# Performance work log

Measured on AMD Instinct MI355X. Metric: run time of the kernel, lower is better.

Reference implementation:

```python
import jax, jax.numpy as jnp
import numpy as np
import math

B, S, T = 128, 600, 200
ENC = 512      # listener_hidden_size * 2
P = 128        # projection_size (hardcoded 128 in forward)
E = 256        # embedding_dim
H = 512        # hidden_dim
V = 31         # vocab_size
SOS = 1


def setup_inputs() -> dict:
    key = jax.random.key(0)
    ks = iter(jax.random.split(key, 40))
    def rn(shape, scale):
        return (jax.random.normal(next(ks), shape, dtype=jnp.float32) * scale)
    inp = {}
    inp['x'] = rn((B, S, ENC), 1.0)
    inp['y'] = jax.random.randint(next(ks), (B, T), 0, V)
    inp['enc_lens'] = jax.random.randint(next(ks), (B,), 100, S + 1)
    # xavier-normal initial hidden/cell states (as in the torch forward)
    xav = math.sqrt(2.0 / (B + H))
    inp['h0'] = rn((3, B, H), xav)
    inp['c0'] = rn((3, B, H), xav)
    # embedding, padding_idx=0 row zeroed
    emb = rn((V, E), 0.05)
    inp['emb'] = emb.at[0].set(0.0)
    # LSTM cells: cell0 input E+P, cells 1,2 input H. torch init: U(-1/sqrt(H), 1/sqrt(H))
    def uni(shape):
        lim = 1.0 / math.sqrt(H)
        return jax.random.uniform(next(ks), shape, jnp.float32, -lim, lim)
    inp['W_ih0'] = uni((4 * H, E + P)); inp['W_hh0'] = uni((4 * H, H))
    inp['b_ih0'] = uni((4 * H,));       inp['b_hh0'] = uni((4 * H,))
    inp['W_ih1'] = uni((4 * H, H));     inp['W_hh1'] = uni((4 * H, H))
    inp['b_ih1'] = uni((4 * H,));       inp['b_hh1'] = uni((4 * H,))
    inp['W_ih2'] = uni((4 * H, H));     inp['W_hh2'] = uni((4 * H, H))
    inp['b_ih2'] = uni((4 * H,));       inp['b_hh2'] = uni((4 * H,))
    # attention projections
    inp['KW_w'] = rn((P, ENC), 0.03); inp['KW_b'] = jnp.zeros((P,), jnp.float32)
    inp['VW_w'] = rn((P, ENC), 0.03); inp['VW_b'] = jnp.zeros((P,), jnp.float32)
    inp['QW_w'] = rn((P, H), 0.03);   inp['QW_b'] = jnp.zeros((P,), jnp.float32)
    # CDN head
    inp['out_w'] = rn((E, H + P), 0.03); inp['out_b'] = jnp.zeros((E,), jnp.float32)
    inp['char_w'] = rn((V, E), 0.05);    inp['char_b'] = jnp.zeros((V,), jnp.float32)
    return inp


def _lstm_cell(x, h, c, W_ih, W_hh, b_ih, b_hh):
    g = x @ W_ih.T + b_ih + h @ W_hh.T + b_hh
    i, f, gg, o = jnp.split(g, 4, axis=-1)
    c = jax.nn.sigmoid(f) * c + jax.nn.sigmoid(i) * jnp.tanh(gg)
    h = jax.nn.sigmoid(o) * jnp.tanh(c)
    return h, c


def reference(x, y, enc_lens, h0, c0, emb,
              W_ih0, W_hh0, b_ih0, b_hh0,
              W_ih1, W_hh1, b_ih1, b_hh1,
              W_ih2, W_hh2, b_ih2, b_hh2,
              KW_w, KW_b, VW_w, VW_b, QW_w, QW_b,
              out_w, out_b, char_w, char_b):
    # set_key_value
    key_ = x @ KW_w.T + KW_b      # (B,S,P)
    value = x @ VW_w.T + VW_b     # (B,S,P)
    mask = jnp.arange(S)[None, :] >= enc_lens[:, None]  # (B,S) True = masked
    scale = 1.0 / math.sqrt(P)

    cells = ((W_ih0, W_hh0, b_ih0, b_hh0),
             (W_ih1, W_hh1, b_ih1, b_hh1),
             (W_ih2, W_hh2, b_ih2, b_hh2))

    # teacher forcing ratio 1: input token at step t is SOS (t=0) then y[:, t-1]
    tokens = jnp.concatenate([jnp.full((B, 1), SOS, dtype=y.dtype), y[:, :-1]], axis=1)
    tokens = tokens.T  # (T,B)

    def step(carry, tok):
        hs, cs, ctx = carry
        inp = jnp.concatenate([emb[tok], ctx], axis=1)  # (B, E+P)
        new_h, new_c = [], []
        for i in range(3):
            h, c = _lstm_cell(inp, hs[i], cs[i], *cells[i])
            new_h.append(h); new_c.append(c)
            inp = h
        rnn_out = inp  # (B,H)
        q = rnn_out @ QW_w.T + QW_b                              # (B,P)
        logits = jnp.einsum('bsp,bp->bs', key_, q) * scale       # (B,S)
        logits = jnp.where(mask, -jnp.inf, logits)
        w = jax.nn.softmax(logits, axis=1)                        # (B,S)
        ctx = jnp.einsum('bs,bsp->bp', w, value)                  # (B,P)
        cdn_in = jnp.concatenate([rnn_out, ctx], axis=1)          # (B,H+P)
        hidden = jax.nn.gelu(cdn_in @ out_w.T + out_b, approximate=False)
        pred = hidden @ char_w.T + char_b                         # (B,V)
        return (jnp.stack(new_h), jnp.stack(new_c), ctx), (pred, w)

    ctx0 = jnp.zeros((B, P), dtype=x.dtype)
    _, (preds, attn) = jax.lax.scan(step, (h0, c0, ctx0), tokens)
    raw_outputs = jnp.transpose(preds, (1, 0, 2))      # (B,T,V)
    attention_plot = jnp.transpose(attn, (1, 0, 2))    # (B,T,S)
    return raw_outputs, attention_plot
```

## Files before the change

### kernel.cpp

```cpp
#include <hip/hip_runtime.h>
#include <hip/hip_fp16.h>


#define Bc 128
#define Sc 600
#define Tc 200
#define ENCc 512
#define Pc 128
#define Ec 256
#define Hc 512
#define Vc 31

__device__ __forceinline__ float sigmoidf_(float x) { return 1.f / (1.f + expf(-x)); }

__global__ __launch_bounds__(256) void init_kernel(
    const float* __restrict__ h0, const float* __restrict__ c0,
    float* __restrict__ hbuf, float* __restrict__ cst, float* __restrict__ ctx)
{
  const int i = blockIdx.x * 256 + threadIdx.x;
  if (i < 3 * Bc * Hc) { hbuf[i] = h0[i]; cst[i] = c0[i]; }
  if (i < Bc * Pc) ctx[i] = 0.f;
}

__global__ __launch_bounds__(256) void kv_kernel(
    const float* __restrict__ x,
    const float* __restrict__ KW_w, const float* __restrict__ KW_b,
    const float* __restrict__ VW_w, const float* __restrict__ VW_b,
    __half* __restrict__ key16, __half* __restrict__ val16)
{
  const int r0 = blockIdx.x * 32;
  const int tid = threadIdx.x;
  const bool isv = tid >= 128;
  const int p = tid & 127;
  const float* __restrict__ W = isv ? VW_w : KW_w;
  float acc[32];
#pragma unroll
  for (int r = 0; r < 32; ++r) acc[r] = 0.f;
  __shared__ float xs[32][64];
  for (int c = 0; c < 8; ++c) {
    const int k0 = c * 64;
    __syncthreads();
#pragma unroll
    for (int i = 0; i < 2; ++i) {
      const int e = i * 256 + tid;
      const int row = e >> 4, c4 = e & 15;
      *(float4*)(&xs[row][c4 * 4]) =
          *(const float4*)(x + (size_t)(r0 + row) * ENCc + k0 + c4 * 4);
    }
    __syncthreads();
    const float* wr = W + (size_t)p * ENCc + k0;
#pragma unroll
    for (int kk = 0; kk < 16; ++kk) {
      const float4 w4 = *(const float4*)(wr + kk * 4);
#pragma unroll
      for (int r = 0; r < 32; ++r) {
        const float4 xv = *(const float4*)(&xs[r][kk * 4]);
        acc[r] += w4.x * xv.x + w4.y * xv.y + w4.z * xv.z + w4.w * xv.w;
      }
    }
  }
  const float bias = isv ? VW_b[p] : KW_b[p];
  __half* __restrict__ dst = isv ? val16 : key16;
#pragma unroll
  for (int r = 0; r < 32; ++r)
    dst[(size_t)(r0 + r) * Pc + p] = __float2half(acc[r] + bias);
}

#define CHUNK_COMPUTE(W0_, W1_, W2_, W3_, K0_)                                   \
  {                                                                              \
    _Pragma("unroll") for (int m = 0; m < 4; ++m)                                \
    {                                                                            \
      const int kl = kg * 4 + m * 32;                                            \
      const float4 a0 = *(const float4*)((W0_) + (K0_) + kl);                    \
      const float4 a1 = *(const float4*)((W1_) + (K0_) + kl);                    \
      const float4 a2 = *(const float4*)((W2_) + (K0_) + kl);                    \
      const float4 a3 = *(const float4*)((W3_) + (K0_) + kl);                    \
      _Pragma("unroll") for (int bb = 0; bb < 4; ++bb)                           \
      {                                                                          \
        const float4 xv = *(const float4*)(&xs[bq * 4 + bb][kl]);                \
        acc[0][bb] += a0.x * xv.x + a0.y * xv.y + a0.z * xv.z + a0.w * xv.w;     \
        acc[1][bb] += a1.x * xv.x + a1.y * xv.y + a1.z * xv.z + a1.w * xv.w;     \
        acc[2][bb] += a2.x * xv.x + a2.y * xv.y + a2.z * xv.z + a2.w * xv.w;     \
        acc[3][bb] += a3.x * xv.x + a3.y * xv.y + a3.z * xv.z + a3.w * xv.w;     \
      }                                                                          \
    }                                                                            \
  }

template <int CELL>
__global__ __launch_bounds__(512) void cell_kernel(
    const float* __restrict__ W_ih, const float* __restrict__ W_hh,
    const float* __restrict__ b_ih, const float* __restrict__ b_hh,
    const float* __restrict__ emb, const int* __restrict__ y,
    const float* __restrict__ ctx,
    const float* __restrict__ hold, float* __restrict__ hnew,
    float* __restrict__ cst, const int t)
{
  constexpr int K1 = (CELL == 0) ? 384 : 512;
  const int u0 = blockIdx.x * 8, b0 = blockIdx.y * 32;
  const int tid = threadIdx.x;
  const int kg = tid & 7, bq = (tid >> 3) & 7, jq = tid >> 6;
  const int u = u0 + jq;
  float acc[4][4] = {{0.f,0.f,0.f,0.f},{0.f,0.f,0.f,0.f},{0.f,0.f,0.f,0.f},{0.f,0.f,0.f,0.f}};
  __shared__ float xs[32][132];

  {
    const float* w0 = W_ih + (size_t)(u)        * K1;
    const float* w1 = W_ih + (size_t)(u + 512)  * K1;
    const float* w2 = W_ih + (size_t)(u + 1024) * K1;
    const float* w3 = W_ih + (size_t)(u + 1536) * K1;
#pragma unroll
    for (int c = 0; c < K1 / 128; ++c) {
      const int k0 = c * 128;
      __syncthreads();
#pragma unroll
      for (int i = 0; i < 2; ++i) {
        const int e = i * 512 + tid;
        const int row = e >> 5, c4 = e & 31;
        const int k = k0 + c4 * 4;
        const int b = b0 + row;
        float4 v;
        if (CELL == 0) {
          if (k < 256) {
            const int tok = (t == 0) ? 1 : y[b * Tc + t - 1];
            v = *(const float4*)(emb + (size_t)tok * Ec + k);
          } else {
            v = *(const float4*)(ctx + (size_t)b * Pc + (k - 256));
          }
        } else {
          v = *(const float4*)(hnew + (size_t)(CELL - 1) * (Bc * Hc) + (size_t)b * Hc + k);
        }
        *(float4*)(&xs[row][c4 * 4]) = v;
      }
      __syncthreads();
      CHUNK_COMPUTE(w0, w1, w2, w3, k0)
    }
  }
  {
    const float* w0 = W_hh + (size_t)(u)        * Hc;
    const float* w1 = W_hh + (size_t)(u + 512)  * Hc;
    const float* w2 = W_hh + (size_t)(u + 1024) * Hc;
    const float* w3 = W_hh + (size_t)(u + 1536) * Hc;
    const float* hsrc = hold + (size_t)CELL * (Bc * Hc);
#pragma unroll
    for (int c = 0; c < 4; ++c) {
      const int k0 = c * 128;
      __syncthreads();
#pragma unroll
      for (int i = 0; i < 2; ++i) {
        const int e = i * 512 + tid;
        const int row = e >> 5, c4 = e & 31;
        *(float4*)(&xs[row][c4 * 4]) =
            *(const float4*)(hsrc + (size_t)(b0 + row) * Hc + k0 + c4 * 4);
      }
      __syncthreads();
      CHUNK_COMPUTE(w0, w1, w2, w3, k0)
    }
  }
#pragma unroll
  for (int g = 0; g < 4; ++g) {
#pragma unroll
    for (int bb = 0; bb < 4; ++bb) {
      float v = acc[g][bb];
      v += __shfl_xor(v, 1);
      v += __shfl_xor(v, 2);
      v += __shfl_xor(v, 4);
      acc[g][bb] = v;
    }
  }
  if (kg == 0) {
    const float bi = b_ih[u]        + b_hh[u];
    const float bf = b_ih[u + 512]  + b_hh[u + 512];
    const float bg = b_ih[u + 1024] + b_hh[u + 1024];
    const float bo = b_ih[u + 1536] + b_hh[u + 1536];
    float* hn = hnew + (size_t)CELL * (Bc * Hc);
    float* cs = cst  + (size_t)CELL * (Bc * Hc);
#pragma unroll
    for (int bb = 0; bb < 4; ++bb) {
      const int b = b0 + bq * 4 + bb;
      const int idx = b * Hc + u;
      const float ig = sigmoidf_(acc[0][bb] + bi);
      const float fg = sigmoidf_(acc[1][bb] + bf);
      const float gg = tanhf(acc[2][bb] + bg);
      const float og = sigmoidf_(acc[3][bb] + bo);
      const float cn = fg * cs[idx] + ig * gg;
      cs[idx] = cn;
      hn[idx] = og * tanhf(cn);
    }
  }
}

__device__ __forceinline__ float wave_max_(float v) {
#pragma unroll
  for (int o = 32; o; o >>= 1) v = fmaxf(v, __shfl_xor(v, o));
  return v;
}
__device__ __forceinline__ float wave_sum_(float v) {
#pragma unroll
  for (int o = 32; o; o >>= 1) v += __shfl_xor(v, o);
  return v;
}

__global__ __launch_bounds__(256) void attn_cdn_kernel(
    const float* __restrict__ hnew,
    const __half* __restrict__ key16, const __half* __restrict__ val16,
    const int* __restrict__ enc_lens,
    const float* __restrict__ QW_w, const float* __restrict__ QW_b,
    const float* __restrict__ out_w, const float* __restrict__ out_b,
    const float* __restrict__ char_w, const float* __restrict__ char_b,
    float* __restrict__ ctx_out, float* __restrict__ raw_out,
    float* __restrict__ attn_out, const int t)
{
  const int b = blockIdx.x, tid = threadIdx.x;
  __shared__ float h2s[Hc], qs[Pc], wsm[Sc], ctxs[Pc], hid[Ec];
  __shared__ float s_red[4];
  const float* h2 = hnew + 2 * (Bc * Hc) + (size_t)b * Hc;
  for (int i = tid; i < Hc; i += 256) h2s[i] = h2[i];
  __syncthreads();
  if (tid < Pc) {
    const float* wr = QW_w + (size_t)tid * Hc;
    float a = QW_b[tid];
#pragma unroll 8
    for (int k = 0; k < Hc; k += 4) {
      const float4 w = *(const float4*)(wr + k);
      a += w.x * h2s[k] + w.y * h2s[k + 1] + w.z * h2s[k + 2] + w.w * h2s[k + 3];
    }
    qs[tid] = a;
  }
  __syncthreads();
  const int len = enc_lens[b];
  float lmax = -3.0e38f;
  for (int s = tid; s < Sc; s += 256) {
    if (s < len) {
      const __half* kr = key16 + ((size_t)(b * Sc + s)) * Pc;
      float a = 0.f;
#pragma unroll 16
      for (int p = 0; p < Pc; p += 4) {
        const float2 k01 = __half22float2(*(const __half2*)(kr + p));
        const float2 k23 = __half22float2(*(const __half2*)(kr + p + 2));
        a += k01.x * qs[p] + k01.y * qs[p + 1] + k23.x * qs[p + 2] + k23.y * qs[p + 3];
      }
      const float sc = a * 0.08838834764831845f;
      wsm[s] = sc;
      lmax = fmaxf(lmax, sc);
    }
  }
  float wm = wave_max_(lmax);
  if ((tid & 63) == 0) s_red[tid >> 6] = wm;
  __syncthreads();
  const float mx = fmaxf(fmaxf(s_red[0], s_red[1]), fmaxf(s_red[2], s_red[3]));
  __syncthreads();
  float lsum = 0.f;
  for (int s = tid; s < Sc; s += 256)
    if (s < len) { const float e = expf(wsm[s] - mx); wsm[s] = e; lsum += e; }
  float ws_ = wave_sum_(lsum);
  if ((tid & 63) == 0) s_red[tid >> 6] = ws_;
  __syncthreads();
  const float inv = 1.f / (s_red[0] + s_red[1] + s_red[2] + s_red[3]);
  float* ap = attn_out + ((size_t)(b * Tc + t)) * Sc;
  for (int s = tid; s < Sc; s += 256) {
    const float w = (s < len) ? wsm[s] * inv : 0.f;
    wsm[s] = w;
    ap[s] = w;
  }
  __syncthreads();
  if (tid < Pc) {
    const __half* vp = val16 + ((size_t)b * Sc) * Pc + tid;
    float a = 0.f;
#pragma unroll 4
    for (int s = 0; s < len; ++s) a += wsm[s] * __half2float(vp[(size_t)s * Pc]);
    ctxs[tid] = a;
    ctx_out[b * Pc + tid] = a;
  }
  __syncthreads();
  {
    const float* wr = out_w + (size_t)tid * (Hc + Pc);
    float a = out_b[tid];
#pragma unroll 8
    for (int k = 0; k < Hc; k += 4) {
      const float4 w = *(const float4*)(wr + k);
      a += w.x * h2s[k] + w.y * h2s[k + 1] + w.z * h2s[k + 2] + w.w * h2s[k + 3];
    }
#pragma unroll 8
    for (int k = 0; k < Pc; k += 4) {
      const float4 w = *(const float4*)(wr + Hc + k);
      a += w.x * ctxs[k] + w.y * ctxs[k + 1] + w.z * ctxs[k + 2] + w.w * ctxs[k + 3];
    }
    hid[tid] = 0.5f * a * (1.f + erff(a * 0.70710678118654752440f));
  }
  __syncthreads();
  if (tid < Vc) {
    const float* wr = char_w + (size_t)tid * Ec;
    float a = char_b[tid];
#pragma unroll 8
    for (int k = 0; k < Ec; k += 4) {
      const float4 w = *(const float4*)(wr + k);
      a += w.x * hid[k] + w.y * hid[k + 1] + w.z * hid[k + 2] + w.w * hid[k + 3];
    }
    raw_out[((size_t)(b * Tc + t)) * Vc + tid] = a;
  }
}

extern "C" void kernel_launch(void* const* d_in, const int* in_sizes, int n_in,
                              void* d_out, int out_size, void* d_ws, size_t ws_size,
                              hipStream_t stream) {
  (void)in_sizes; (void)n_in; (void)out_size; (void)ws_size;
  const float* x      = (const float*)d_in[0];
  const int*   y      = (const int*)  d_in[1];
  const int*   enc    = (const int*)  d_in[2];
  const float* h0     = (const float*)d_in[3];
  const float* c0     = (const float*)d_in[4];
  const float* emb    = (const float*)d_in[5];
  const float* W_ih0  = (const float*)d_in[6];
  const float* W_hh0  = (const float*)d_in[7];
  const float* b_ih0  = (const float*)d_in[8];
  const float* b_hh0  = (const float*)d_in[9];
  const float* W_ih1  = (const float*)d_in[10];
  const float* W_hh1  = (const float*)d_in[11];
  const float* b_ih1  = (const float*)d_in[12];
  const float* b_hh1  = (const float*)d_in[13];
  const float* W_ih2  = (const float*)d_in[14];
  const float* W_hh2  = (const float*)d_in[15];
  const float* b_ih2  = (const float*)d_in[16];
  const float* b_hh2  = (const float*)d_in[17];
  const float* KW_w   = (const float*)d_in[18];
  const float* KW_b   = (const float*)d_in[19];
  const float* VW_w   = (const float*)d_in[20];
  const float* VW_b   = (const float*)d_in[21];
  const float* QW_w   = (const float*)d_in[22];
  const float* QW_b   = (const float*)d_in[23];
  const float* out_w  = (const float*)d_in[24];
  const float* out_b  = (const float*)d_in[25];
  const float* char_w = (const float*)d_in[26];
  const float* char_b = (const float*)d_in[27];

  float* out  = (float*)d_out;
  float* raw  = out;
  float* attn = out + 793600;

  char* ws = (char*)d_ws;
  __half* key16 = (__half*)(ws);
  __half* val16 = (__half*)(ws + 19660800);
  float*  hbuf  = (float*) (ws + 39321600);
  float*  cst   = (float*) (ws + 39321600 + 1572864);
  float*  ctx   = (float*) (ws + 39321600 + 1572864 + 786432);

  init_kernel<<<768, 256, 0, stream>>>(h0, c0, hbuf, cst, ctx);
  kv_kernel<<<2400, 256, 0, stream>>>(x, KW_w, KW_b, VW_w, VW_b, key16, val16);

  for (int t = 0; t < Tc; ++t) {
    float* hold = hbuf + (size_t)(t & 1) * (3 * Bc * Hc);
    float* hnew = hbuf + (size_t)((t & 1) ^ 1) * (3 * Bc * Hc);
    cell_kernel<0><<<dim3(64, 4), 512, 0, stream>>>(W_ih0, W_hh0, b_ih0, b_hh0,
                                                    emb, y, ctx, hold, hnew, cst, t);
    cell_kernel<1><<<dim3(64, 4), 512, 0, stream>>>(W_ih1, W_hh1, b_ih1, b_hh1,
                                                    emb, y, ctx, hold, hnew, cst, t);
    cell_kernel<2><<<dim3(64, 4), 512, 0, stream>>>(W_ih2, W_hh2, b_ih2, b_hh2,
                                                    emb, y, ctx, hold, hnew, cst, t);
    attn_cdn_kernel<<<128, 256, 0, stream>>>(hnew, key16, val16, enc,
                                             QW_w, QW_b, out_w, out_b, char_w, char_b,
                                             ctx, raw, attn, t);
  }
}
```

Baseline: 30.94 ms.

## Fuse per-timestep cell and attention launches into one persistent cooperative kernel

Replaces the 800 per-timestep kernel launches with a single cooperative persistent kernel of 256 blocks. The blocks step through the three LSTM cells and the attention/CDN phase, separated by a hand-rolled flag-based grid barrier. The layer-0 input (embedding plus context) is now built into a staging buffer by idle blocks during the attention phase, and the attention block size doubles to 512 threads with the context reduction split over two halves. The aim is to remove launch overhead and gaps between kernels. In exchange it adds spin-wait barrier latency and depends on all 256 blocks being co-resident.

```diff
diff --git a/kernel.cpp b/kernel.cpp
--- a/kernel.cpp
+++ b/kernel.cpp
@@ -10,16 +10,23 @@
 #define Ec 256
 #define Hc 512
 #define Vc 31
+#define BHc (Bc * Hc)
 
 __device__ __forceinline__ float sigmoidf_(float x) { return 1.f / (1.f + expf(-x)); }
 
 __global__ __launch_bounds__(256) void init_kernel(
     const float* __restrict__ h0, const float* __restrict__ c0,
-    float* __restrict__ hbuf, float* __restrict__ cst, float* __restrict__ ctx)
+    const float* __restrict__ emb,
+    float* __restrict__ hbuf, float* __restrict__ cst,
+    float* __restrict__ xin0, unsigned* __restrict__ bar)
 {
   const int i = blockIdx.x * 256 + threadIdx.x;
-  if (i < 3 * Bc * Hc) { hbuf[i] = h0[i]; cst[i] = c0[i]; }
-  if (i < Bc * Pc) ctx[i] = 0.f;
+  if (i < 3 * BHc) { hbuf[i] = h0[i]; cst[i] = c0[i]; }
+  if (i < Bc * 384) {
+    const int k = i % 384;
+    xin0[i] = (k < 256) ? emb[256 + k] : 0.f;
+  }
+  if (i < 257) bar[i] = 0u;
 }
 
 __global__ __launch_bounds__(256) void kv_kernel(
@@ -64,6 +71,26 @@
 #pragma unroll
   for (int r = 0; r < 32; ++r)
     dst[(size_t)(r0 + r) * Pc + p] = __float2half(acc[r] + bias);
+}
+
+__device__ __forceinline__ void grid_bar(unsigned* __restrict__ arrive,
+                                         unsigned* __restrict__ go, unsigned it) {
+  __syncthreads();
+  if (threadIdx.x == 0)
+    __hip_atomic_store(&arrive[blockIdx.x], it, __ATOMIC_RELEASE, __HIP_MEMORY_SCOPE_AGENT);
+  if (blockIdx.x == 0) {
+    if (threadIdx.x < 256) {
+      while (__hip_atomic_load(&arrive[threadIdx.x], __ATOMIC_ACQUIRE,
+                               __HIP_MEMORY_SCOPE_AGENT) < it) {}
+    }
+    __syncthreads();
+    if (threadIdx.x == 0)
+      __hip_atomic_store(go, it, __ATOMIC_RELEASE, __HIP_MEMORY_SCOPE_AGENT);
+  }
+  if (threadIdx.x == 0) {
+    while (__hip_atomic_load(go, __ATOMIC_ACQUIRE, __HIP_MEMORY_SCOPE_AGENT) < it) {}
+  }
+  __syncthreads();
 }
 
 #define CHUNK_COMPUTE(W0_, W1_, W2_, W3_, K0_)                                   \
@@ -86,22 +113,20 @@
     }                                                                            \
   }
 
-template <int CELL>
-__global__ __launch_bounds__(512) void cell_kernel(
+template <int K1>
+__device__ __forceinline__ void cell_phase(
     const float* __restrict__ W_ih, const float* __restrict__ W_hh,
     const float* __restrict__ b_ih, const float* __restrict__ b_hh,
-    const float* __restrict__ emb, const int* __restrict__ y,
-    const float* __restrict__ ctx,
+    const float* __restrict__ xin,
     const float* __restrict__ hold, float* __restrict__ hnew,
-    float* __restrict__ cst, const int t)
+    float* __restrict__ cs, float* __restrict__ smem)
 {
-  constexpr int K1 = (CELL == 0) ? 384 : 512;
-  const int u0 = blockIdx.x * 8, b0 = blockIdx.y * 32;
+  const int u0 = (blockIdx.x >> 2) * 8, b0 = (blockIdx.x & 3) * 32;
   const int tid = threadIdx.x;
   const int kg = tid & 7, bq = (tid >> 3) & 7, jq = tid >> 6;
   const int u = u0 + jq;
   float acc[4][4] = {{0.f,0.f,0.f,0.f},{0.f,0.f,0.f,0.f},{0.f,0.f,0.f,0.f},{0.f,0.f,0.f,0.f}};
-  __shared__ float xs[32][132];
+  float (*xs)[132] = (float (*)[132])smem;
 
   {
     const float* w0 = W_ih + (size_t)(u)        * K1;
@@ -116,20 +141,8 @@
       for (int i = 0; i < 2; ++i) {
         const int e = i * 512 + tid;
         const int row = e >> 5, c4 = e & 31;
-        const int k = k0 + c4 * 4;
-        const int b = b0 + row;
-        float4 v;
-        if (CELL == 0) {
-          if (k < 256) {
-            const int tok = (t == 0) ? 1 : y[b * Tc + t - 1];
-            v = *(const float4*)(emb + (size_t)tok * Ec + k);
-          } else {
-            v = *(const float4*)(ctx + (size_t)b * Pc + (k - 256));
-          }
-        } else {
-          v = *(const float4*)(hnew + (size_t)(CELL - 1) * (Bc * Hc) + (size_t)b * Hc + k);
-        }
-        *(float4*)(&xs[row][c4 * 4]) = v;
+        *(float4*)(&xs[row][c4 * 4]) =
+            *(const float4*)(xin + (size_t)(b0 + row) * K1 + k0 + c4 * 4);
       }
       __syncthreads();
       CHUNK_COMPUTE(w0, w1, w2, w3, k0)
@@ -140,7 +153,6 @@
     const float* w1 = W_hh + (size_t)(u + 512)  * Hc;
     const float* w2 = W_hh + (size_t)(u + 1024) * Hc;
     const float* w3 = W_hh + (size_t)(u + 1536) * Hc;
-    const float* hsrc = hold + (size_t)CELL * (Bc * Hc);
 #pragma unroll
     for (int c = 0; c < 4; ++c) {
       const int k0 = c * 128;
@@ -150,7 +162,7 @@
         const int e = i * 512 + tid;
         const int row = e >> 5, c4 = e & 31;
         *(float4*)(&xs[row][c4 * 4]) =
-            *(const float4*)(hsrc + (size_t)(b0 + row) * Hc + k0 + c4 * 4);
+            *(const float4*)(hold + (size_t)(b0 + row) * Hc + k0 + c4 * 4);
       }
       __syncthreads();
       CHUNK_COMPUTE(w0, w1, w2, w3, k0)
@@ -172,8 +184,6 @@
     const float bf = b_ih[u + 512]  + b_hh[u + 512];
     const float bg = b_ih[u + 1024] + b_hh[u + 1024];
     const float bo = b_ih[u + 1536] + b_hh[u + 1536];
-    float* hn = hnew + (size_t)CELL * (Bc * Hc);
-    float* cs = cst  + (size_t)CELL * (Bc * Hc);
 #pragma unroll
     for (int bb = 0; bb < 4; ++bb) {
       const int b = b0 + bq * 4 + bb;
@@ -184,7 +194,7 @@
       const float og = sigmoidf_(acc[3][bb] + bo);
       const float cn = fg * cs[idx] + ig * gg;
       cs[idx] = cn;
-      hn[idx] = og * tanhf(cn);
+      hnew[idx] = og * tanhf(cn);
     }
   }
 }
@@ -200,21 +210,37 @@
   return v;
 }
 
-__global__ __launch_bounds__(256) void attn_cdn_kernel(
-    const float* __restrict__ hnew,
+__device__ __forceinline__ void attn_phase(
+    const float* __restrict__ h2,
     const __half* __restrict__ key16, const __half* __restrict__ val16,
     const int* __restrict__ enc_lens,
     const float* __restrict__ QW_w, const float* __restrict__ QW_b,
     const float* __restrict__ out_w, const float* __restrict__ out_b,
     const float* __restrict__ char_w, const float* __restrict__ char_b,
-    float* __restrict__ ctx_out, float* __restrict__ raw_out,
-    float* __restrict__ attn_out, const int t)
+    const float* __restrict__ emb, const int* __restrict__ y,
+    float* __restrict__ xin0,
+    float* __restrict__ raw_out, float* __restrict__ attn_out,
+    float* __restrict__ smem, const int t)
 {
-  const int b = blockIdx.x, tid = threadIdx.x;
-  __shared__ float h2s[Hc], qs[Pc], wsm[Sc], ctxs[Pc], hid[Ec];
-  __shared__ float s_red[4];
-  const float* h2 = hnew + 2 * (Bc * Hc) + (size_t)b * Hc;
-  for (int i = tid; i < Hc; i += 256) h2s[i] = h2[i];
+  const int tid = threadIdx.x;
+  if (blockIdx.x >= 128) {
+    const int b = blockIdx.x - 128;
+    if (tid < 256) {
+      const int tok = y[b * Tc + t];
+      xin0[b * 384 + tid] = emb[tok * Ec + tid];
+    }
+    return;
+  }
+  const int b = blockIdx.x;
+  float* h2s  = smem;
+  float* qs   = smem + 512;
+  float* wsm  = smem + 640;
+  float* ctxs = smem + 1240;
+  float* hid  = smem + 1368;
+  float* red  = smem + 1632;
+  float* part = smem + 1648;
+
+  h2s[tid] = h2[(size_t)b * Hc + tid];
   __syncthreads();
   if (tid < Pc) {
     const float* wr = QW_w + (size_t)tid * Hc;
@@ -229,7 +255,7 @@
   __syncthreads();
   const int len = enc_lens[b];
   float lmax = -3.0e38f;
-  for (int s = tid; s < Sc; s += 256) {
+  for (int s = tid; s < Sc; s += 512) {
     if (s < len) {
       const __half* kr = key16 + ((size_t)(b * Sc + s)) * Pc;
       float a = 0.f;
@@ -245,34 +271,47 @@
     }
   }
   float wm = wave_max_(lmax);
-  if ((tid & 63) == 0) s_red[tid >> 6] = wm;
-  __syncthreads();
-  const float mx = fmaxf(fmaxf(s_red[0], s_red[1]), fmaxf(s_red[2], s_red[3]));
+  if ((tid & 63) == 0) red[tid >> 6] = wm;
+  __syncthreads();
+  float mx = red[0];
+#pragma unroll
+  for (int w = 1; w < 8; ++w) mx = fmaxf(mx, red[w]);
   __syncthreads();
   float lsum = 0.f;
-  for (int s = tid; s < Sc; s += 256)
+  for (int s = tid; s < Sc; s += 512)
     if (s < len) { const float e = expf(wsm[s] - mx); wsm[s] = e; lsum += e; }
   float ws_ = wave_sum_(lsum);
-  if ((tid & 63) == 0) s_red[tid >> 6] = ws_;
-  __syncthreads();
-  const float inv = 1.f / (s_red[0] + s_red[1] + s_red[2] + s_red[3]);
+  if ((tid & 63) == 0) red[tid >> 6] = ws_;
+  __syncthreads();
+  float tot = 0.f;
+#pragma unroll
+  for (int w = 0; w < 8; ++w) tot += red[w];
+  const float inv = 1.f / tot;
   float* ap = attn_out + ((size_t)(b * Tc + t)) * Sc;
-  for (int s = tid; s < Sc; s += 256) {
+  for (int s = tid; s < Sc; s += 512) {
     const float w = (s < len) ? wsm[s] * inv : 0.f;
     wsm[s] = w;
     ap[s] = w;
   }
   __syncthreads();
-  if (tid < Pc) {
-    const __half* vp = val16 + ((size_t)b * Sc) * Pc + tid;
+  if (tid < 256) {
+    const int p = tid & 127, hf = tid >> 7;
+    const int s_beg = hf * 300;
+    const int s_end = (len < (hf + 1) * 300) ? ((len > s_beg) ? len : s_beg) : (hf + 1) * 300;
+    const __half* vp = val16 + ((size_t)b * Sc) * Pc + p;
     float a = 0.f;
 #pragma unroll 4
-    for (int s = 0; s < len; ++s) a += wsm[s] * __half2float(vp[(size_t)s * Pc]);
+    for (int s = s_beg; s < s_end; ++s) a += wsm[s] * __half2float(vp[(size_t)s * Pc]);
+    part[hf * 128 + p] = a;
+  }
+  __syncthreads();
+  if (tid < Pc) {
+    const float a = part[tid] + part[128 + tid];
     ctxs[tid] = a;
-    ctx_out[b * Pc + tid] = a;
-  }
-  __syncthreads();
-  {
+    xin0[b * 384 + 256 + tid] = a;
+  }
+  __syncthreads();
+  if (tid < Ec) {
     const float* wr = out_w + (size_t)tid * (Hc + Pc);
     float a = out_b[tid];
 #pragma unroll 8
@@ -297,6 +336,40 @@
       a += w.x * hid[k] + w.y * hid[k + 1] + w.z * hid[k + 2] + w.w * hid[k + 3];
     }
     raw_out[((size_t)(b * Tc + t)) * Vc + tid] = a;
+  }
+}
+
+struct PParams {
+  const float *W_ih0, *W_hh0, *b_ih0, *b_hh0;
+  const float *W_ih1, *W_hh1, *b_ih1, *b_hh1;
+  const float *W_ih2, *W_hh2, *b_ih2, *b_hh2;
+  const float *emb; const int *y; const int *enc;
+  const float *QW_w, *QW_b, *out_w, *out_b, *char_w, *char_b;
+  const __half *key16, *val16;
+  float *hbuf, *cst, *xin0;
+  unsigned *bar_arrive, *bar_go;
+  float *raw, *attn;
+};
+
+__global__ __launch_bounds__(512, 2) void persist_kernel(PParams p) {
+  __shared__ float smem[32 * 132];
+  unsigned it = 0;
+  for (int t = 0; t < Tc; ++t) {
+    const float* hold = p.hbuf + (size_t)(t & 1) * (3 * BHc);
+    float* hnew = p.hbuf + (size_t)((t & 1) ^ 1) * (3 * BHc);
+    cell_phase<384>(p.W_ih0, p.W_hh0, p.b_ih0, p.b_hh0, p.xin0,
+                    hold, hnew, p.cst, smem);
+    grid_bar(p.bar_arrive, p.bar_go, ++it);
+    cell_phase<512>(p.W_ih1, p.W_hh1, p.b_ih1, p.b_hh1, hnew,
+                    hold + BHc, hnew + BHc, p.cst + BHc, smem);
+    grid_bar(p.bar_arrive, p.bar_go, ++it);
+    cell_phase<512>(p.W_ih2, p.W_hh2, p.b_ih2, p.b_hh2, hnew + BHc,
+                    hold + 2 * BHc, hnew + 2 * BHc, p.cst + 2 * BHc, smem);
+    grid_bar(p.bar_arrive, p.bar_go, ++it);
+    attn_phase(hnew + 2 * BHc, p.key16, p.val16, p.enc, p.QW_w, p.QW_b,
+               p.out_w, p.out_b, p.char_w, p.char_b, p.emb, p.y,
+               p.xin0, p.raw, p.attn, smem, t);
+    grid_bar(p.bar_arrive, p.bar_go, ++it);
   }
 }
 
@@ -338,26 +411,29 @@
   float* attn = out + 793600;
 
   char* ws = (char*)d_ws;
-  __half* key16 = (__half*)(ws);
-  __half* val16 = (__half*)(ws + 19660800);
-  float*  hbuf  = (float*) (ws + 39321600);
-  float*  cst   = (float*) (ws + 39321600 + 1572864);
-  float*  ctx   = (float*) (ws + 39321600 + 1572864 + 786432);
-
-  init_kernel<<<768, 256, 0, stream>>>(h0, c0, hbuf, cst, ctx);
+  __half*   key16 = (__half*)(ws);
+  __half*   val16 = (__half*)(ws + 19660800);
+  float*    hbuf  = (float*)(ws + 39321600);
+  float*    cst   = (float*)(ws + 39321600 + 1572864);
+  float*    xin0  = (float*)(ws + 39321600 + 1572864 + 786432);
+  unsigned* bar   = (unsigned*)(ws + 39321600 + 1572864 + 786432 + 196608);
+
+  init_kernel<<<768, 256, 0, stream>>>(h0, c0, emb, hbuf, cst, xin0, bar);
   kv_kernel<<<2400, 256, 0, stream>>>(x, KW_w, KW_b, VW_w, VW_b, key16, val16);
 
-  for (int t = 0; t < Tc; ++t) {
-    float* hold = hbuf + (size_t)(t & 1) * (3 * Bc * Hc);
-    float* hnew = hbuf + (size_t)((t & 1) ^ 1) * (3 * Bc * Hc);
-    cell_kernel<0><<<dim3(64, 4), 512, 0, stream>>>(W_ih0, W_hh0, b_ih0, b_hh0,
-                                                    emb, y, ctx, hold, hnew, cst, t);
-    cell_kernel<1><<<dim3(64, 4), 512, 0, stream>>>(W_ih1, W_hh1, b_ih1, b_hh1,
-                                                    emb, y, ctx, hold, hnew, cst, t);
-    cell_kernel<2><<<dim3(64, 4), 512, 0, stream>>>(W_ih2, W_hh2, b_ih2, b_hh2,
-                                                    emb, y, ctx, hold, hnew, cst, t);
-    attn_cdn_kernel<<<128, 256, 0, stream>>>(hnew, key16, val16, enc,
-                                             QW_w, QW_b, out_w, out_b, char_w, char_b,
-                                             ctx, raw, attn, t);
-  }
-}
+  PParams p;
+  p.W_ih0 = W_ih0; p.W_hh0 = W_hh0; p.b_ih0 = b_ih0; p.b_hh0 = b_hh0;
+  p.W_ih1 = W_ih1; p.W_hh1 = W_hh1; p.b_ih1 = b_ih1; p.b_hh1 = b_hh1;
+  p.W_ih2 = W_ih2; p.W_hh2 = W_hh2; p.b_ih2 = b_ih2; p.b_hh2 = b_hh2;
+  p.emb = emb; p.y = y; p.enc = enc;
+  p.QW_w = QW_w; p.QW_b = QW_b; p.out_w = out_w; p.out_b = out_b;
+  p.char_w = char_w; p.char_b = char_b;
+  p.key16 = key16; p.val16 = val16;
+  p.hbuf = hbuf; p.cst = cst; p.xin0 = xin0;
+  p.bar_arrive = bar; p.bar_go = bar + 256;
+  p.raw = raw; p.attn = attn;
+
+  void* args[] = { &p };
+  hipLaunchCooperativeKernel((const void*)persist_kernel, dim3(256), dim3(512),
+                             args, 0, stream);
+}
```

Result: slower. 83.81 ms (+170.9%).
